# Kernel optimization log

Measured on AMD Instinct MI355X. Metric: run time of the kernel, lower is better.

## Reference

```python
import jax, jax.numpy as jnp
import numpy as np

NLAT, NLON = 256, 512
LMAX, MMAX = 256, 257  # legendre-gauss: lmax=nlat, mmax=nlon//2+1
BATCH, CHAN = 16, 8


def setup_inputs() -> dict:
    key = jax.random.key(0)
    kx, kw = jax.random.split(key)
    # vector field on the sphere: [..., 2 (theta/phi components), nlat, nlon]
    x = jax.random.normal(kx, (BATCH, CHAN, 2, NLAT, NLON), dtype=jnp.float32)
    # precomputed Legendre-derivative quadrature weights [2, mmax, lmax, nlat]
    # (stands in for precompute_dlegpoly * quad weights * 1/(l(l+1)), with weights[1] sign flip folded in)
    weights = 0.02 * jax.random.normal(kw, (2, MMAX, LMAX, NLAT), dtype=jnp.float32)
    return {"x": x, "weights": weights}


def reference(x, weights):
    # forward rfft over longitude, scaled by 2*pi (norm='forward' divides by nlon)
    xf = (2.0 * jnp.pi) * jnp.fft.rfft(x, axis=-1, norm="forward")  # [..., 2, nlat, nfreq] complex
    mmax = weights.shape[1]
    xf = xf[..., :mmax]
    # split vector components and real/imag parts
    xt = xf[..., 0, :, :]  # theta component [..., nlat, mmax]
    xp = xf[..., 1, :, :]  # phi component
    xtr, xti = jnp.real(xt), jnp.imag(xt)
    xpr, xpi = jnp.real(xp), jnp.imag(xp)
    w0 = weights[0]  # [mmax, lmax, nlat]
    w1 = weights[1]

    def contract(a, w):
        # batched per-m matmul: [..., k, m] x [m, l, k] -> [..., l, m]
        return jnp.einsum("...km,mlk->...lm", a, w)

    # spheroidal (component 0) and toroidal (component 1) coefficients
    out0 = (contract(xtr, w0) - contract(xpi, w1)) + 1j * (contract(xti, w0) + contract(xpr, w1))
    out1 = (-contract(xti, w1) - contract(xpr, w0)) + 1j * (contract(xtr, w1) - contract(xpi, w0))
    return jnp.stack([out0, out1], axis=-3)  # [..., 2, lmax, mmax] complex64
```

## Files before the change

### kernel.cpp

```cpp
#include <hip/hip_runtime.h>
#include <hip/hip_bf16.h>
#include <math.h>

#define NLAT 256
#define NLON 512
#define LMAX 256
#define MMAX 257
#define BC   128

#define X_ELEMS 33554432
#define W_ELEMS 33685504
#define W_BYTES (W_ELEMS * 4LL)

#define FM    288
#define F_BYTES  ((size_t)2*FM*512*2)
#define A_BYTES  ((size_t)4*BC*MMAX*NLAT*2)
#define OUTS_BYTES ((size_t)MMAX*2*BC*LMAX*2)

typedef short bf16x8 __attribute__((ext_vector_type(8)));
typedef float f32x4  __attribute__((ext_vector_type(4)));

__device__ __forceinline__ unsigned int bfpack2(float a, float b) {
    unsigned short lo = __builtin_bit_cast(unsigned short, __float2bfloat16(a));
    unsigned short hi = __builtin_bit_cast(unsigned short, __float2bfloat16(b));
    return (unsigned int)lo | ((unsigned int)hi << 16);
}
__device__ __forceinline__ unsigned short bf16bits(float a) {
    return __builtin_bit_cast(unsigned short, __float2bfloat16(a));
}
__device__ __forceinline__ void gload16(const void* g, void* l) {
    __builtin_amdgcn_global_load_lds(
        (const __attribute__((address_space(1))) unsigned int*)g,
        (__attribute__((address_space(3))) unsigned int*)l, 16, 0, 0);
}

__global__ __launch_bounds__(256) void f_init(unsigned short* __restrict__ F)
{
    int mm = blockIdx.x, o = blockIdx.y, t = threadIdx.x;
    const float s = 6.283185307179586f / 512.0f;
    for (int c = 0; c < 2; ++c) {
        int n = t * 2 + c;
        float val = 0.0f;
        if (mm < MMAX) {
            int j = (mm * n) & 511;
            float ang = 6.283185307179586f * (float)j / 512.0f;
            float sn, cs; __sincosf(ang, &sn, &cs);
            val = (o == 0) ? s * cs : -s * sn;
        }
        F[((size_t)o * FM + mm) * 512 + n] =
            __builtin_bit_cast(unsigned short, __float2bfloat16(val));
    }
}

__global__ __launch_bounds__(512, 1) void dft_mfma(const float* __restrict__ x,
                                                   const unsigned short* __restrict__ F,
                                                   unsigned short* __restrict__ aout)
{
    __shared__ __align__(16) unsigned char fl[2][32768];
    unsigned char* xl = (unsigned char*)fl;

    int bcc = blockIdx.x;
    int kh  = blockIdx.y;
    int bc = bcc >> 1, comp = bcc & 1;
    int t = threadIdx.x;
    int wid = t >> 6, lane = t & 63;

    int o = wid >> 2, kt = wid & 3;
    int r15 = lane & 15, hi = lane >> 4;
    int klocal = kt * 16 + r15;
    unsigned braw = (unsigned)klocal * 1024u;
    unsigned bswz = (unsigned)(klocal & 15) << 4;

    bf16x8 barr0[16], barr1[16];
    #pragma unroll
    for (int s = 0; s < 2; ++s) {
        const float* xg = x + ((size_t)bcc * NLAT + kh * 128 + s * 64) * NLON;
        #pragma unroll
        for (int p = 0; p < 8; ++p) {
            int row = wid * 8 + p;
            const float* src = xg + (size_t)row * NLON + lane * 8;
            float4 f0 = *(const float4*)(src);
            float4 f1 = *(const float4*)(src + 4);
            uint4 v;
            v.x = bfpack2(f0.x, f0.y); v.y = bfpack2(f0.z, f0.w);
            v.z = bfpack2(f1.x, f1.y); v.w = bfpack2(f1.z, f1.w);
            unsigned off = ((unsigned)row * 1024u + (unsigned)lane * 16u)
                           ^ ((unsigned)(row & 15) << 4);
            *(uint4*)(xl + off) = v;
        }
        __syncthreads();
        #pragma unroll
        for (int nt = 0; nt < 16; ++nt) {
            unsigned c0 = (unsigned)(nt * 64 + hi * 16);
            bf16x8 v = *(const bf16x8*)(xl + ((braw + c0) ^ bswz));
            if (s == 0) barr0[nt] = v; else barr1[nt] = v;
        }
        __syncthreads();
    }

    const unsigned char* Fb = (const unsigned char*)F;
    unsigned gcol = ((unsigned)lane * 16u);

    #define STAGE_F(buf, mt)                                                  \
        {                                                                     \
            _Pragma("unroll")                                                 \
            for (int p = 0; p < 4; ++p) {                                     \
                int fr = wid * 4 + p;                                         \
                int o2 = fr >> 4, mr = fr & 15;                               \
                size_t grow = (size_t)o2 * FM + (mt) * 16 + mr;               \
                const void* g = Fb + grow * 1024u                             \
                                + (gcol ^ ((unsigned)(fr & 15) << 4));        \
                gload16(g, (unsigned char*)fl[buf] + (unsigned)fr * 1024u);   \
            }                                                                 \
        }

    STAGE_F(0, 0);
    __syncthreads();

    unsigned arow = (unsigned)(o * 16 + r15);
    unsigned abase = arow * 1024u;
    unsigned aswz = (unsigned)r15 << 4;
    unsigned short* ao = aout;
    int v = comp * 2 + o;

    for (int mt = 0; mt < 17; ++mt) {
        int cur = mt & 1;
        if (mt < 16) STAGE_F(cur ^ 1, mt + 1);

        const unsigned char* fb = fl[cur];
        f32x4 accA0 = {0.f,0.f,0.f,0.f}, accA1 = {0.f,0.f,0.f,0.f};
        f32x4 accB0 = {0.f,0.f,0.f,0.f}, accB1 = {0.f,0.f,0.f,0.f};
        #pragma unroll
        for (int nt = 0; nt < 16; nt += 2) {
            unsigned c0 = (unsigned)(nt * 64 + hi * 16);
            bf16x8 a0 = *(const bf16x8*)(fb + ((abase + c0)       ^ aswz));
            bf16x8 a1 = *(const bf16x8*)(fb + ((abase + c0 + 64u) ^ aswz));
            accA0 = __builtin_amdgcn_mfma_f32_16x16x32_bf16(a0, barr0[nt],     accA0, 0, 0, 0);
            accB0 = __builtin_amdgcn_mfma_f32_16x16x32_bf16(a0, barr1[nt],     accB0, 0, 0, 0);
            accA1 = __builtin_amdgcn_mfma_f32_16x16x32_bf16(a1, barr0[nt + 1], accA1, 0, 0, 0);
            accB1 = __builtin_amdgcn_mfma_f32_16x16x32_bf16(a1, barr1[nt + 1], accB1, 0, 0, 0);
        }
        #pragma unroll
        for (int j = 0; j < 4; ++j) {
            accA0[j] += accA1[j];
            accB0[j] += accB1[j];
        }

        #pragma unroll
        for (int j = 0; j < 4; ++j) {
            int mm0 = mt * 16 + hi * 4 + j;
            if (mm0 < MMAX) {
                size_t base = (((size_t)v * BC + bc) * MMAX + mm0) * NLAT + kh * 128;
                ao[base + klocal]      = bf16bits(accA0[j]);
                ao[base + klocal + 64] = bf16bits(accB0[j]);
            }
        }
        __syncthreads();
    }
    #undef STAGE_F
}

template <int MODE>
__global__ __launch_bounds__(512, 1) void contract_mfma(const unsigned short* __restrict__ a,
                                                        const float* __restrict__ w,
                                                        void* __restrict__ outv)
{
    __shared__ __align__(16) unsigned char Ab[2][32768];
    __shared__ __align__(16) unsigned char Bb[2][20480];
    int m  = blockIdx.x;
    int lh = blockIdx.y;
    int t = threadIdx.x;
    int wid = t >> 6, lane = t & 63;
    int o = wid >> 2, h = (wid >> 1) & 1, q = wid & 1;
    int r15 = lane & 15, hi = lane >> 4;
    int l0 = lh * 128;

    f32x4 accLo[4][4] = {};
    f32x4 accHi[4][4] = {};

    int bcr = t >> 2, ch4 = t & 3;
    int lB  = t >> 2, chB = t & 3;

    #define STAGE_A2(buf, ii)                                                   \
        {                                                                       \
            int ph_ = (ii) >> 2;                                                \
            _Pragma("unroll")                                                   \
            for (int sub = 0; sub < 2; ++sub) {                                 \
                int k0_ = (((ii) & 3) * 2 + sub) * 32;                          \
                _Pragma("unroll")                                               \
                for (int i = 0; i < 2; ++i) {                                   \
                    int vsel = (i == 0) ? (ph_ ? 3 : 0) : (ph_ ? 1 : 2);        \
                    const void* g = a + (((size_t)vsel * BC + bcr) * MMAX + m) * NLAT \
                                      + k0_ + (ch4 ^ (bcr & 3)) * 8;            \
                    gload16(g, Ab[buf] + sub * 16384 + i * 8192 + wid * 1024);  \
                }                                                               \
            }                                                                   \
        }

    float4 wr[4];
    #define WLOAD2(ii)                                                          \
        {                                                                       \
            int ph_ = (ii) >> 2;                                                \
            _Pragma("unroll")                                                   \
            for (int sub = 0; sub < 2; ++sub) {                                 \
                int k0_ = (((ii) & 3) * 2 + sub) * 32;                          \
                const float* wp = w + (((size_t)ph_ * MMAX + m) * LMAX + l0 + lB) * NLAT \
                                    + k0_ + chB * 8;                            \
                wr[sub * 2]     = *(const float4*)(wp);                         \
                wr[sub * 2 + 1] = *(const float4*)(wp + 4);                     \
            }                                                                   \
        }
    #define BWRITE2(buf)                                                        \
        {                                                                       \
            _Pragma("unroll")                                                   \
            for (int sub = 0; sub < 2; ++sub) {                                 \
                uint4 vv;                                                       \
                vv.x = bfpack2(wr[sub * 2].x,     wr[sub * 2].y);               \
                vv.y = bfpack2(wr[sub * 2].z,     wr[sub * 2].w);               \
                vv.z = bfpack2(wr[sub * 2 + 1].x, wr[sub * 2 + 1].y);           \
                vv.w = bfpack2(wr[sub * 2 + 1].z, wr[sub * 2 + 1].w);           \
                *(uint4*)(Bb[buf] + sub * 10240 + lB * 80 + chB * 16) = vv;     \
            }                                                                   \
        }
    #define MFMA_PHASE2(ACC)                                                    \
        {                                                                       \
            _Pragma("unroll")                                                   \
            for (int sub = 0; sub < 2; ++sub) {                                 \
                const unsigned char* bbs = bb + sub * 10240;                    \
                const unsigned char* abs_ = ab + sub * 16384;                   \
                bf16x8 bfr[4];                                                  \
                _Pragma("unroll")                                               \
                for (int lt = 0; lt < 4; ++lt)                                  \
                    bfr[lt] = *(const bf16x8*)(bbs + (q * 64 + lt * 16 + r15) * 80 + hi * 16); \
                _Pragma("unroll")                                               \
                for (int bt = 0; bt < 4; ++bt) {                                \
                    bf16x8 af = *(const bf16x8*)(abs_ + (o * 128 + h * 64 + bt * 16 + r15) * 64 \
                                                   + ((hi * 16) ^ ((r15 & 3) << 4))); \
                    _Pragma("unroll")                                           \
                    for (int lt = 0; lt < 4; ++lt)                              \
                        ACC[bt][lt] = __builtin_amdgcn_mfma_f32_16x16x32_bf16(af, bfr[lt], ACC[bt][lt], 0, 0, 0); \
                }                                                               \
            }                                                                   \
        }

    STAGE_A2(0, 0);
    WLOAD2(0);
    __syncthreads();
    BWRITE2(0);

    for (int ii = 0; ii < 8; ++ii) {
        int cur = ii & 1;
        if (ii < 7) WLOAD2(ii + 1);
        __syncthreads();
        if (ii < 7) STAGE_A2(cur ^ 1, ii + 1);

        const unsigned char* bb = Bb[cur];
        const unsigned char* ab = Ab[cur];
        if (ii < 4) MFMA_PHASE2(accLo) else MFMA_PHASE2(accHi);

        if (ii < 7) BWRITE2(cur ^ 1);
    }

    #pragma unroll
    for (int bt = 0; bt < 4; ++bt) {
        #pragma unroll
        for (int lt = 0; lt < 4; ++lt) {
            #pragma unroll
            for (int j = 0; j < 4; ++j) {
                int bc = h * 64 + bt * 16 + hi * 4 + j;
                int l  = l0 + q * 64 + lt * 16 + r15;
                float lo = accLo[bt][lt][j];
                float hh = accHi[bt][lt][j];
                float val = (o == 0) ? (lo - hh) : (0.0f - (lo + hh));
                if (MODE == 0) {
                    __hip_bfloat16* outs = (__hip_bfloat16*)outv;
                    outs[(((size_t)m * 2 + o) * BC + bc) * LMAX + l] = __float2bfloat16(val);
                } else {
                    float* out = (float*)outv;
                    out[(((size_t)bc * 2 + o) * LMAX + l) * MMAX + m] = val;
                }
            }
        }
    }
    #undef STAGE_A2
    #undef WLOAD2
    #undef BWRITE2
    #undef MFMA_PHASE2
}

__global__ __launch_bounds__(256) void transpose_out(const unsigned short* __restrict__ outs,
                                                     float* __restrict__ out)
{
    __shared__ float tile[32][65];
    int mt = blockIdx.x;
    int lt = blockIdx.y;
    int z  = blockIdx.z;
    int bc = z >> 1, o = z & 1;
    int t = threadIdx.x;

    {
        int r = t >> 3, c0 = (t & 7) * 8;
        int mm = mt * 32 + r;
        if (mm < MMAX) {
            const unsigned short* src = outs + (((size_t)mm * 2 + o) * BC + bc) * LMAX + lt * 64 + c0;
            uint4 v = *(const uint4*)src;
            const unsigned short* u = (const unsigned short*)&v;
            #pragma unroll
            for (int i = 0; i < 8; ++i)
                tile[r][c0 + i] = __bfloat162float(__builtin_bit_cast(__hip_bfloat16, u[i]));
        }
    }
    __syncthreads();
    {
        int l = t >> 2, mc = (t & 3) * 8;
        float* dst = out + (((size_t)bc * 2 + o) * LMAX + lt * 64 + l) * MMAX + mt * 32 + mc;
        #pragma unroll
        for (int i = 0; i < 8; ++i) {
            int mm = mt * 32 + mc + i;
            if (mm < MMAX) dst[i] = tile[mc + i][l];
        }
    }
}

#define PER_BC ((size_t)4 * MMAX * NLAT * sizeof(__hip_bfloat16))

__global__ __launch_bounds__(256) void dft_legacy(const float* __restrict__ x,
                                                  __hip_bfloat16* __restrict__ a,
                                                  int bc0, int nbc)
{
    __shared__ float  xs[512];
    __shared__ float2 tw[512];
    int t = threadIdx.x;
    int b = blockIdx.x;
    int lat = b & (NLAT - 1);
    int comp = (b >> 8) & 1;
    int bcl = b >> 9;
    int bc = bc0 + bcl;
    const float* xr = x + (((size_t)bc * 2 + comp) * NLAT + lat) * NLON;
    for (int j = t; j < 512; j += 256) {
        xs[j] = xr[j];
        float ang = -6.283185307179586f * (float)j / 512.0f;
        float sn, cs; sincosf(ang, &sn, &cs);
        tw[j] = make_float2(cs, sn);
    }
    __syncthreads();
    const float scale = 6.283185307179586f / 512.0f;
    size_t VS = (size_t)nbc * MMAX * NLAT;
    __hip_bfloat16* p0 = a + (size_t)(comp * 2) * VS + (size_t)bcl * MMAX * NLAT + lat;
    __hip_bfloat16* p1 = p0 + VS;
    for (int m = t; m < MMAX; m += 256) {
        float accr = 0.f, acci = 0.f;
        int j = 0;
        for (int n = 0; n < 512; ++n) {
            float xv = xs[n]; float2 wv = tw[j];
            accr += xv * wv.x; acci += xv * wv.y;
            j = (j + m) & 511;
        }
        p0[(size_t)m * NLAT] = __float2bfloat16(accr * scale);
        p1[(size_t)m * NLAT] = __float2bfloat16(acci * scale);
    }
}

__global__ __launch_bounds__(256) void contract_legacy(const __hip_bfloat16* __restrict__ a,
                                                       const float* __restrict__ w,
                                                       float* __restrict__ out,
                                                       int bc0, int nbc)
{
    __shared__ float w0s[16][NLAT + 1];
    __shared__ float w1s[16][NLAT + 1];
    __shared__ float as[4][4][NLAT + 1];
    __shared__ float2 red2[256];
    int tid = threadIdx.x;
    int m = blockIdx.x, l0 = blockIdx.y * 16, bct = blockIdx.z * 4;
    const float* w0g = w + ((size_t)m * LMAX + l0) * NLAT;
    const float* w1g = w0g + (size_t)MMAX * LMAX * NLAT;
    for (int idx = tid; idx < 16 * NLAT; idx += 256) {
        int l = idx >> 8, k = idx & 255;
        w0s[l][k] = w0g[(size_t)l * NLAT + k];
        w1s[l][k] = w1g[(size_t)l * NLAT + k];
    }
    size_t VS = (size_t)nbc * MMAX * NLAT;
    for (int idx = tid; idx < 4 * 4 * NLAT; idx += 256) {
        int v = idx >> 10, bl = (idx >> 8) & 3, k = idx & 255;
        int bls = bct + bl; if (bls > nbc - 1) bls = nbc - 1;
        as[v][bl][k] = __bfloat162float(a[(size_t)v * VS + ((size_t)bls * MMAX + m) * NLAT + k]);
    }
    __syncthreads();
    int l = tid & 15, b = (tid >> 4) & 3, kseg = tid >> 6;
    float acc0 = 0.f, acc2 = 0.f;
    int kbeg = kseg * 64;
    #pragma unroll 8
    for (int k = kbeg; k < kbeg + 64; ++k) {
        float tr = as[0][b][k], ti = as[1][b][k], pr = as[2][b][k], pi = as[3][b][k];
        float w0 = w0s[l][k], w1 = w1s[l][k];
        acc0 += tr * w0 - pi * w1;
        acc2 -= ti * w1 + pr * w0;
    }
    red2[tid] = make_float2(acc0, acc2);
    __syncthreads();
    if (kseg == 0 && (bct + b) < nbc) {
        #pragma unroll
        for (int s = 1; s < 4; ++s) {
            float2 r = red2[tid + 64 * s];
            acc0 += r.x; acc2 += r.y;
        }
        int bc = bc0 + bct + b;
        out[(((size_t)bc * 2 + 0) * LMAX + (l0 + l)) * MMAX + m] = acc0;
        out[(((size_t)bc * 2 + 1) * LMAX + (l0 + l)) * MMAX + m] = acc2;
    }
}

extern "C" void kernel_launch(void* const* d_in, const int* in_sizes, int n_in,
                              void* d_out, int out_size, void* d_ws, size_t ws_size,
                              hipStream_t stream)
{
    const float* x = (const float*)d_in[0];
    const float* w = (const float*)d_in[1];
    if (n_in >= 2) {
        long long s0 = (long long)in_sizes[0];
        if (s0 == (long long)W_ELEMS || s0 == W_BYTES) {
            w = (const float*)d_in[0];
            x = (const float*)d_in[1];
        }
    }
    float* out = (float*)d_out;

    if (ws_size >= F_BYTES + A_BYTES) {
        unsigned short* F = (unsigned short*)d_ws;
        unsigned short* a = (unsigned short*)((char*)d_ws + F_BYTES);
        hipLaunchKernelGGL(f_init, dim3(FM, 2), dim3(256), 0, stream, F);
        hipLaunchKernelGGL(dft_mfma, dim3(256, 2), dim3(512), 0, stream, x, F, a);
        if (ws_size >= F_BYTES + A_BYTES + OUTS_BYTES) {
            unsigned short* outs = (unsigned short*)((char*)d_ws + F_BYTES + A_BYTES);
            hipLaunchKernelGGL((contract_mfma<0>), dim3(MMAX, 2), dim3(512), 0, stream,
                               a, w, (void*)outs);
            hipLaunchKernelGGL(transpose_out, dim3(9, 4, 256), dim3(256), 0, stream,
                               outs, out);
        } else {
            hipLaunchKernelGGL((contract_mfma<1>), dim3(MMAX, 2), dim3(512), 0, stream,
                               a, w, (void*)out);
        }
    } else {
        __hip_bfloat16* a = (__hip_bfloat16*)d_ws;
        int nbc = 1;
        for (int c = 128; c >= 1; c >>= 1)
            if (PER_BC * (size_t)c <= ws_size) { nbc = c; break; }
        int nchunks = BC / nbc;
        for (int cc = 0; cc < nchunks; ++cc) {
            int bc0 = cc * nbc;
            hipLaunchKernelGGL(dft_legacy, dim3(nbc * 2 * NLAT), dim3(256), 0, stream,
                               x, a, bc0, nbc);
            hipLaunchKernelGGL(contract_legacy, dim3(MMAX, LMAX / 16, (nbc + 3) / 4),
                               dim3(256), 0, stream, a, w, out, bc0, nbc);
        }
    }
}
```

Baseline: 192.0 us.

## Fold sign into a negated A plane and process full L range per block

The DFT kernel now also writes a negated copy of one spectral plane (a fifth plane), so the contraction can accumulate both phases into one accumulator instead of keeping separate Lo/Hi accumulators and combining them with a subtraction. The contraction kernel now covers all 256 l values per block, so the grid drops from MMAX x 2 to MMAX blocks and each A tile staged in LDS is reused across both l halves. In exchange it needs more workspace and extra DFT writes, doubles the B tile in LDS, and keeps more accumulator registers live. Under-utilization is a risk, since 257 blocks of 512 threads may leave many CUs idle.

```diff
diff --git a/kernel.cpp b/kernel.cpp
--- a/kernel.cpp
+++ b/kernel.cpp
@@ -14,7 +14,9 @@
 
 #define FM    288
 #define F_BYTES  ((size_t)2*FM*512*2)
-#define A_BYTES  ((size_t)4*BC*MMAX*NLAT*2)
+#define PS    ((size_t)BC*MMAX*NLAT)
+#define A4_BYTES ((size_t)4*PS*2)
+#define A5_BYTES ((size_t)5*PS*2)
 #define OUTS_BYTES ((size_t)MMAX*2*BC*LMAX*2)
 
 typedef short bf16x8 __attribute__((ext_vector_type(8)));
@@ -54,7 +56,8 @@
 
 __global__ __launch_bounds__(512, 1) void dft_mfma(const float* __restrict__ x,
                                                    const unsigned short* __restrict__ F,
-                                                   unsigned short* __restrict__ aout)
+                                                   unsigned short* __restrict__ aout,
+                                                   int write5)
 {
     __shared__ __align__(16) unsigned char fl[2][32768];
     unsigned char* xl = (unsigned char*)fl;
@@ -122,6 +125,7 @@
     unsigned aswz = (unsigned)r15 << 4;
     unsigned short* ao = aout;
     int v = comp * 2 + o;
+    int wantneg = (write5 && v == 3);
 
     for (int mt = 0; mt < 17; ++mt) {
         int cur = mt & 1;
@@ -153,6 +157,11 @@
                 size_t base = (((size_t)v * BC + bc) * MMAX + mm0) * NLAT + kh * 128;
                 ao[base + klocal]      = bf16bits(accA0[j]);
                 ao[base + klocal + 64] = bf16bits(accB0[j]);
+                if (wantneg) {
+                    size_t nb = base + PS;
+                    ao[nb + klocal]      = bf16bits(-accA0[j]);
+                    ao[nb + klocal + 64] = bf16bits(-accB0[j]);
+                }
             }
         }
         __syncthreads();
@@ -161,22 +170,19 @@
 }
 
 template <int MODE>
-__global__ __launch_bounds__(512, 1) void contract_mfma(const unsigned short* __restrict__ a,
-                                                        const float* __restrict__ w,
-                                                        void* __restrict__ outv)
+__global__ __launch_bounds__(512, 1) void contract_v9(const unsigned short* __restrict__ a,
+                                                      const float* __restrict__ w,
+                                                      void* __restrict__ outv)
 {
     __shared__ __align__(16) unsigned char Ab[2][32768];
-    __shared__ __align__(16) unsigned char Bb[2][20480];
+    __shared__ __align__(16) unsigned char Bb[2][40960];
     int m  = blockIdx.x;
-    int lh = blockIdx.y;
     int t = threadIdx.x;
     int wid = t >> 6, lane = t & 63;
     int o = wid >> 2, h = (wid >> 1) & 1, q = wid & 1;
     int r15 = lane & 15, hi = lane >> 4;
-    int l0 = lh * 128;
-
-    f32x4 accLo[4][4] = {};
-    f32x4 accHi[4][4] = {};
+
+    f32x4 acc[2][4][4] = {};
 
     int bcr = t >> 2, ch4 = t & 3;
     int lB  = t >> 2, chB = t & 3;
@@ -189,7 +195,7 @@
                 int k0_ = (((ii) & 3) * 2 + sub) * 32;                          \
                 _Pragma("unroll")                                               \
                 for (int i = 0; i < 2; ++i) {                                   \
-                    int vsel = (i == 0) ? (ph_ ? 3 : 0) : (ph_ ? 1 : 2);        \
+                    int vsel = (i == 0) ? (ph_ ? 4 : 0) : (ph_ ? 1 : 2);        \
                     const void* g = a + (((size_t)vsel * BC + bcr) * MMAX + m) * NLAT \
                                       + k0_ + (ch4 ^ (bcr & 3)) * 8;            \
                     gload16(g, Ab[buf] + sub * 16384 + i * 8192 + wid * 1024);  \
@@ -197,48 +203,60 @@
             }                                                                   \
         }
 
-    float4 wr[4];
+    float4 wr[8];
     #define WLOAD2(ii)                                                          \
         {                                                                       \
             int ph_ = (ii) >> 2;                                                \
             _Pragma("unroll")                                                   \
             for (int sub = 0; sub < 2; ++sub) {                                 \
                 int k0_ = (((ii) & 3) * 2 + sub) * 32;                          \
-                const float* wp = w + (((size_t)ph_ * MMAX + m) * LMAX + l0 + lB) * NLAT \
-                                    + k0_ + chB * 8;                            \
-                wr[sub * 2]     = *(const float4*)(wp);                         \
-                wr[sub * 2 + 1] = *(const float4*)(wp + 4);                     \
+                _Pragma("unroll")                                               \
+                for (int lh = 0; lh < 2; ++lh) {                                \
+                    const float* wp = w + (((size_t)ph_ * MMAX + m) * LMAX       \
+                                           + lh * 128 + lB) * NLAT              \
+                                        + k0_ + chB * 8;                        \
+                    wr[(sub * 2 + lh) * 2]     = *(const float4*)(wp);          \
+                    wr[(sub * 2 + lh) * 2 + 1] = *(const float4*)(wp + 4);      \
+                }                                                               \
             }                                                                   \
         }
     #define BWRITE2(buf)                                                        \
         {                                                                       \
             _Pragma("unroll")                                                   \
             for (int sub = 0; sub < 2; ++sub) {                                 \
-                uint4 vv;                                                       \
-                vv.x = bfpack2(wr[sub * 2].x,     wr[sub * 2].y);               \
-                vv.y = bfpack2(wr[sub * 2].z,     wr[sub * 2].w);               \
-                vv.z = bfpack2(wr[sub * 2 + 1].x, wr[sub * 2 + 1].y);           \
-                vv.w = bfpack2(wr[sub * 2 + 1].z, wr[sub * 2 + 1].w);           \
-                *(uint4*)(Bb[buf] + sub * 10240 + lB * 80 + chB * 16) = vv;     \
+                _Pragma("unroll")                                               \
+                for (int lh = 0; lh < 2; ++lh) {                                \
+                    int e = (sub * 2 + lh) * 2;                                 \
+                    uint4 vv;                                                   \
+                    vv.x = bfpack2(wr[e].x,     wr[e].y);                       \
+                    vv.y = bfpack2(wr[e].z,     wr[e].w);                       \
+                    vv.z = bfpack2(wr[e + 1].x, wr[e + 1].y);                   \
+                    vv.w = bfpack2(wr[e + 1].z, wr[e + 1].w);                   \
+                    *(uint4*)(Bb[buf] + sub * 20480 + lh * 10240                \
+                              + lB * 80 + chB * 16) = vv;                       \
+                }                                                               \
             }                                                                   \
         }
-    #define MFMA_PHASE2(ACC)                                                    \
+    #define MFMA_PHASE2()                                                       \
         {                                                                       \
             _Pragma("unroll")                                                   \
             for (int sub = 0; sub < 2; ++sub) {                                 \
-                const unsigned char* bbs = bb + sub * 10240;                    \
                 const unsigned char* abs_ = ab + sub * 16384;                   \
-                bf16x8 bfr[4];                                                  \
                 _Pragma("unroll")                                               \
-                for (int lt = 0; lt < 4; ++lt)                                  \
-                    bfr[lt] = *(const bf16x8*)(bbs + (q * 64 + lt * 16 + r15) * 80 + hi * 16); \
-                _Pragma("unroll")                                               \
-                for (int bt = 0; bt < 4; ++bt) {                                \
-                    bf16x8 af = *(const bf16x8*)(abs_ + (o * 128 + h * 64 + bt * 16 + r15) * 64 \
-                                                   + ((hi * 16) ^ ((r15 & 3) << 4))); \
+                for (int lh = 0; lh < 2; ++lh) {                                \
+                    const unsigned char* bbs = bb + sub * 20480 + lh * 10240;   \
+                    bf16x8 bfr[4];                                              \
                     _Pragma("unroll")                                           \
                     for (int lt = 0; lt < 4; ++lt)                              \
-                        ACC[bt][lt] = __builtin_amdgcn_mfma_f32_16x16x32_bf16(af, bfr[lt], ACC[bt][lt], 0, 0, 0); \
+                        bfr[lt] = *(const bf16x8*)(bbs + (q * 64 + lt * 16 + r15) * 80 + hi * 16); \
+                    _Pragma("unroll")                                           \
+                    for (int bt = 0; bt < 4; ++bt) {                            \
+                        bf16x8 af = *(const bf16x8*)(abs_ + (o * 128 + h * 64 + bt * 16 + r15) * 64 \
+                                                       + ((hi * 16) ^ ((r15 & 3) << 4))); \
+                        _Pragma("unroll")                                       \
+                        for (int lt = 0; lt < 4; ++lt)                          \
+                            acc[lh][bt][lt] = __builtin_amdgcn_mfma_f32_16x16x32_bf16(af, bfr[lt], acc[lh][bt][lt], 0, 0, 0); \
+                    }                                                           \
                 }                                                               \
             }                                                                   \
         }
@@ -256,28 +274,30 @@
 
         const unsigned char* bb = Bb[cur];
         const unsigned char* ab = Ab[cur];
-        if (ii < 4) MFMA_PHASE2(accLo) else MFMA_PHASE2(accHi);
+        MFMA_PHASE2();
 
         if (ii < 7) BWRITE2(cur ^ 1);
     }
 
     #pragma unroll
-    for (int bt = 0; bt < 4; ++bt) {
-        #pragma unroll
-        for (int lt = 0; lt < 4; ++lt) {
+    for (int lh = 0; lh < 2; ++lh) {
+        #pragma unroll
+        for (int bt = 0; bt < 4; ++bt) {
             #pragma unroll
-            for (int j = 0; j < 4; ++j) {
-                int bc = h * 64 + bt * 16 + hi * 4 + j;
-                int l  = l0 + q * 64 + lt * 16 + r15;
-                float lo = accLo[bt][lt][j];
-                float hh = accHi[bt][lt][j];
-                float val = (o == 0) ? (lo - hh) : (0.0f - (lo + hh));
-                if (MODE == 0) {
-                    __hip_bfloat16* outs = (__hip_bfloat16*)outv;
-                    outs[(((size_t)m * 2 + o) * BC + bc) * LMAX + l] = __float2bfloat16(val);
-                } else {
-                    float* out = (float*)outv;
-                    out[(((size_t)bc * 2 + o) * LMAX + l) * MMAX + m] = val;
+            for (int lt = 0; lt < 4; ++lt) {
+                #pragma unroll
+                for (int j = 0; j < 4; ++j) {
+                    int bc = h * 64 + bt * 16 + hi * 4 + j;
+                    int l  = lh * 128 + q * 64 + lt * 16 + r15;
+                    float av = acc[lh][bt][lt][j];
+                    float val = (o == 0) ? av : (0.0f - av);
+                    if (MODE == 0) {
+                        __hip_bfloat16* outs = (__hip_bfloat16*)outv;
+                        outs[(((size_t)m * 2 + o) * BC + bc) * LMAX + l] = __float2bfloat16(val);
+                    } else {
+                        float* out = (float*)outv;
+                        out[(((size_t)bc * 2 + o) * LMAX + l) * MMAX + m] = val;
+                    }
                 }
             }
         }
@@ -425,21 +445,23 @@
     }
     float* out = (float*)d_out;
 
-    if (ws_size >= F_BYTES + A_BYTES) {
+    if (ws_size >= F_BYTES + A5_BYTES + OUTS_BYTES) {
+        unsigned short* F = (unsigned short*)d_ws;
+        unsigned short* a = (unsigned short*)((char*)d_ws + F_BYTES);
+        unsigned short* outs = (unsigned short*)((char*)d_ws + F_BYTES + A5_BYTES);
+        hipLaunchKernelGGL(f_init, dim3(FM, 2), dim3(256), 0, stream, F);
+        hipLaunchKernelGGL(dft_mfma, dim3(256, 2), dim3(512), 0, stream, x, F, a, 1);
+        hipLaunchKernelGGL((contract_v9<0>), dim3(MMAX), dim3(512), 0, stream,
+                           a, w, (void*)outs);
+        hipLaunchKernelGGL(transpose_out, dim3(9, 4, 256), dim3(256), 0, stream,
+                           outs, out);
+    } else if (ws_size >= F_BYTES + A5_BYTES) {
         unsigned short* F = (unsigned short*)d_ws;
         unsigned short* a = (unsigned short*)((char*)d_ws + F_BYTES);
         hipLaunchKernelGGL(f_init, dim3(FM, 2), dim3(256), 0, stream, F);
-        hipLaunchKernelGGL(dft_mfma, dim3(256, 2), dim3(512), 0, stream, x, F, a);
-        if (ws_size >= F_BYTES + A_BYTES + OUTS_BYTES) {
-            unsigned short* outs = (unsigned short*)((char*)d_ws + F_BYTES + A_BYTES);
-            hipLaunchKernelGGL((contract_mfma<0>), dim3(MMAX, 2), dim3(512), 0, stream,
-                               a, w, (void*)outs);
-            hipLaunchKernelGGL(transpose_out, dim3(9, 4, 256), dim3(256), 0, stream,
-                               outs, out);
-        } else {
-            hipLaunchKernelGGL((contract_mfma<1>), dim3(MMAX, 2), dim3(512), 0, stream,
-                               a, w, (void*)out);
-        }
+        hipLaunchKernelGGL(dft_mfma, dim3(256, 2), dim3(512), 0, stream, x, F, a, 1);
+        hipLaunchKernelGGL((contract_v9<1>), dim3(MMAX), dim3(512), 0, stream,
+                           a, w, (void*)out);
     } else {
         __hip_bfloat16* a = (__hip_bfloat16*)d_ws;
         int nbc = 1;
```

New measurement: 198.1 us. +3.2%, slower.
